# Optimization experiments

Hardware: AMD Instinct MI355X
Metric: run time of the kernel (lower is better)

Reference implementation:

```python
import jax, jax.numpy as jnp
import numpy as np

STD = 0.5      # wrapper's self.std used as the noise sampling std
EPS = 1e-12    # BERT LayerNorm eps
NOISE_SEED = 42


def setup_inputs() -> dict:
    key = jax.random.key(0)
    ks = jax.random.split(key, 8)
    B, S, H, V, P, T = 32, 512, 768, 30522, 512, 2
    return {
        "input_ids": jax.random.randint(ks[0], (B, S), 0, V, dtype=jnp.int32),
        "token_type_ids": jnp.zeros((B, S), dtype=jnp.int32),
        "importance_scores": jax.random.uniform(ks[1], (B, S), dtype=jnp.float32),
        "word_emb": jax.random.normal(ks[2], (V, H), dtype=jnp.float32) * 0.02,
        "pos_emb": jax.random.normal(ks[3], (P, H), dtype=jnp.float32) * 0.02,
        "type_emb": jax.random.normal(ks[4], (T, H), dtype=jnp.float32) * 0.02,
        "ln_gamma": jnp.ones((H,), dtype=jnp.float32),
        "ln_beta": jnp.zeros((H,), dtype=jnp.float32),
    }


def _layernorm(x, g, b):
    mu = x.mean(-1, keepdims=True)
    var = ((x - mu) ** 2).mean(-1, keepdims=True)
    return (x - mu) * jax.lax.rsqrt(var + EPS) * g + b


def reference(input_ids, token_type_ids, importance_scores, word_emb, pos_emb,
              type_emb, ln_gamma, ln_beta):
    B, S = input_ids.shape
    # BERT embeddings: word + position + token_type, then LayerNorm (dropout=eval/no-op)
    emb = word_emb[input_ids] + pos_emb[:S][None, :, :] + type_emb[token_type_ids]
    x = _layernorm(emb, ln_gamma, ln_beta)  # [B,S,H]

    # min-max normalize importance scores per sequence (inf handled as in original)
    smax = importance_scores.max(axis=1, keepdims=True)
    tmp = jnp.where(jnp.isinf(importance_scores), 99.0, importance_scores)
    smin = tmp.min(axis=1, keepdims=True)
    norm = (importance_scores - smin) / (smax - smin)
    norm = jnp.where(importance_scores.sum() == 0, importance_scores, norm)

    finite = jnp.isfinite(importance_scores)
    score = jnp.where(finite, norm, 0.0)      # -inf positions masked out below
    score = score.at[:, 0].set(1.0)           # CLS token forced to importance 1
    mask = finite.at[:, 0].set(True)

    # soft_suff: sigma = 1 - importance; noise ~ N(0, STD); x += noise * sigma * x
    sigma = (1.0 - score) * mask.astype(x.dtype)          # [B,S]
    noise = jax.random.normal(jax.random.key(NOISE_SEED), x.shape, dtype=x.dtype) * STD
    x = x + noise * sigma[:, :, None] * jax.lax.stop_gradient(x)
    return x
```

## Files before the change

kernel.cpp:

```cpp
#include <hip/hip_runtime.h>
#include <math.h>

#define Hh   768
#define Ss   512
#define Bb   32
#define NTOK (Bb * Ss)
#define NT   192

__device__ __forceinline__ void tfr(unsigned &x0, unsigned &x1, int r) {
  x0 += x1;
  x1 = (x1 << r) | (x1 >> (32 - r));
  x1 ^= x0;
}

__device__ __forceinline__ unsigned tf_bits_0_42(unsigned ctr) {
  const unsigned ks1 = 42u, ks2 = 0x1BD11BF0u;
  unsigned x0 = 0u, x1 = ctr + ks1;
  tfr(x0,x1,13); tfr(x0,x1,15); tfr(x0,x1,26); tfr(x0,x1,6);
  x0 += ks1; x1 += ks2 + 1u;
  tfr(x0,x1,17); tfr(x0,x1,29); tfr(x0,x1,16); tfr(x0,x1,24);
  x0 += ks2; x1 += 2u;
  tfr(x0,x1,13); tfr(x0,x1,15); tfr(x0,x1,26); tfr(x0,x1,6);
  x1 += ks1 + 3u;
  tfr(x0,x1,17); tfr(x0,x1,29); tfr(x0,x1,16); tfr(x0,x1,24);
  x0 += ks1; x1 += ks2 + 4u;
  tfr(x0,x1,13); tfr(x0,x1,15); tfr(x0,x1,26); tfr(x0,x1,6);
  x0 += ks2; x1 += 5u;
  return x0 ^ x1;
}

__device__ __forceinline__ float erfinv_bits(unsigned bits) {
  float f = __uint_as_float((bits >> 9) | 0x3F800000u) - 1.0f;
  const float LO = -0.99999994f;
  float x = fmaxf(LO, fmaf(f, 2.0f, LO));
  float w = -__logf(fmaf(-x, x, 1.0f));
  float p;
  if (w < 5.0f) {
    w -= 2.5f;
    p = 2.81022636e-08f;
    p = fmaf(p, w, 3.43273939e-07f);
    p = fmaf(p, w, -3.5233877e-06f);
    p = fmaf(p, w, -4.39150654e-06f);
    p = fmaf(p, w, 0.00021858087f);
    p = fmaf(p, w, -0.00125372503f);
    p = fmaf(p, w, -0.00417768164f);
    p = fmaf(p, w, 0.246640727f);
    p = fmaf(p, w, 1.50140941f);
  } else {
    w = sqrtf(w) - 3.0f;
    p = -0.000200214257f;
    p = fmaf(p, w, 0.000100950558f);
    p = fmaf(p, w, 0.00134934322f);
    p = fmaf(p, w, -0.00367342844f);
    p = fmaf(p, w, 0.00573950773f);
    p = fmaf(p, w, -0.0076224613f);
    p = fmaf(p, w, 0.00943887047f);
    p = fmaf(p, w, 1.00167406f);
    p = fmaf(p, w, 2.83297682f);
  }
  return p * x;
}

__global__ __launch_bounds__(512) void row_stats_kernel(
    const float* __restrict__ imp, float* __restrict__ ws) {
  int b = blockIdx.x;
  int tid = threadIdx.x;
  float v = imp[b * Ss + tid];
  float vmax = v;
  float vmin = isinf(v) ? 99.0f : v;
  float vsum = v;
  for (int o = 32; o > 0; o >>= 1) {
    vmax = fmaxf(vmax, __shfl_down(vmax, o));
    vmin = fminf(vmin, __shfl_down(vmin, o));
    vsum += __shfl_down(vsum, o);
  }
  __shared__ float smax[8], smin[8], ssum[8];
  int wave = tid >> 6, lane = tid & 63;
  if (lane == 0) { smax[wave] = vmax; smin[wave] = vmin; ssum[wave] = vsum; }
  __syncthreads();
  if (tid == 0) {
    float a = smax[0], m = smin[0], c = ssum[0];
    for (int w = 1; w < 8; ++w) {
      a = fmaxf(a, smax[w]); m = fminf(m, smin[w]); c += ssum[w];
    }
    ws[b] = a; ws[32 + b] = m; ws[64 + b] = c;
  }
}

__global__ __launch_bounds__(NT) void bert_embed_ln_noise_kernel(
    const int* __restrict__ ids, const int* __restrict__ tts,
    const float* __restrict__ imp,
    const float* __restrict__ wemb, const float* __restrict__ pemb,
    const float* __restrict__ temb, const float* __restrict__ gamma,
    const float* __restrict__ beta, const float* __restrict__ stats,
    float* __restrict__ out) {
  const int t = blockIdx.x;
  const int b = t >> 9;
  const int s = t & 511;
  const int tid = threadIdx.x;

  const int id = ids[t];
  const int tt = tts[t];
  const float4 wv = ((const float4*)(wemb + (size_t)id * Hh))[tid];
  const float4 pv = ((const float4*)(pemb + (size_t)s  * Hh))[tid];
  const float4 tv = ((const float4*)(temb + (size_t)tt * Hh))[tid];

  const float e0 = wv.x + pv.x + tv.x;
  const float e1 = wv.y + pv.y + tv.y;
  const float e2 = wv.z + pv.z + tv.z;
  const float e3 = wv.w + pv.w + tv.w;

  const unsigned base = (unsigned)t * Hh + 4u * (unsigned)tid;
  const unsigned r0 = tf_bits_0_42(base);
  const unsigned r1 = tf_bits_0_42(base + 1u);
  const unsigned r2 = tf_bits_0_42(base + 2u);
  const unsigned r3 = tf_bits_0_42(base + 3u);
  const float v0 = erfinv_bits(r0);
  const float v1 = erfinv_bits(r1);
  const float v2 = erfinv_bits(r2);
  const float v3 = erfinv_bits(r3);

  __shared__ float redm[3], redv[3];
  __shared__ float sh_ssc;
  const int wave = tid >> 6, lane = tid & 63;

  float ps = (e0 + e1) + (e2 + e3);
  #pragma unroll
  for (int o = 1; o < 64; o <<= 1) ps += __shfl_xor(ps, o);
  if (lane == 0) redm[wave] = ps;
  __syncthreads();
  const float mu = (redm[0] + redm[1] + redm[2]) * (1.0f / Hh);

  const float d0 = e0 - mu, d1 = e1 - mu, d2 = e2 - mu, d3 = e3 - mu;
  float pvv = (d0 * d0 + d1 * d1) + (d2 * d2 + d3 * d3);
  #pragma unroll
  for (int o = 1; o < 64; o <<= 1) pvv += __shfl_xor(pvv, o);
  if (lane == 0) redv[wave] = pvv;

  if (tid == 0) {
    float total = 0.0f;
    for (int w = 0; w < 32; ++w) total += stats[64 + w];
    const float score = imp[t];
    float sig = 0.0f;
    if (s != 0) {
      const bool fin = isfinite(score);
      const float mx = stats[b], mn = stats[32 + b];
      const float val = (total == 0.0f) ? score : (score - mn) / (mx - mn);
      sig = fin ? (1.0f - val) : 0.0f;
    }
    sh_ssc = sig * 0.70710677f;
  }
  __syncthreads();
  const float var = (redv[0] + redv[1] + redv[2]) * (1.0f / Hh);
  const float rstd = rsqrtf(var + 1e-12f);
  const float ssc = sh_ssc;

  const float4 g4 = ((const float4*)gamma)[tid];
  const float4 b4 = ((const float4*)beta)[tid];
  const float y0 = fmaf(d0 * rstd, g4.x, b4.x);
  const float y1 = fmaf(d1 * rstd, g4.y, b4.y);
  const float y2 = fmaf(d2 * rstd, g4.z, b4.z);
  const float y3 = fmaf(d3 * rstd, g4.w, b4.w);

  float4 o4;
  o4.x = fmaf(v0 * ssc, y0, y0);
  o4.y = fmaf(v1 * ssc, y1, y1);
  o4.z = fmaf(v2 * ssc, y2, y2);
  o4.w = fmaf(v3 * ssc, y3, y3);
  ((float4*)(out + (size_t)t * Hh))[tid] = o4;
}

extern "C" void kernel_launch(void* const* d_in, const int* in_sizes, int n_in,
                              void* d_out, int out_size, void* d_ws, size_t ws_size,
                              hipStream_t stream) {
  const int*   ids   = (const int*)d_in[0];
  const int*   tts   = (const int*)d_in[1];
  const float* imp   = (const float*)d_in[2];
  const float* wemb  = (const float*)d_in[3];
  const float* pemb  = (const float*)d_in[4];
  const float* temb  = (const float*)d_in[5];
  const float* gamma = (const float*)d_in[6];
  const float* beta  = (const float*)d_in[7];
  float* out   = (float*)d_out;
  float* stats = (float*)d_ws;

  row_stats_kernel<<<Bb, Ss, 0, stream>>>(imp, stats);
  bert_embed_ln_noise_kernel<<<NTOK, NT, 0, stream>>>(
      ids, tts, imp, wemb, pemb, temb, gamma, beta, stats, out);
}
```

Baseline: 173.6 us.

## Map one token per wavefront, precompute sigma, and make erfinv branchless

Restructures the main kernel so each 64-lane wavefront handles a whole token (12 elements per lane), packing four tokens per 256-thread block. LayerNorm reductions then use only wave shuffles, with no shared memory or __syncthreads. Per-token sigma moves into a separate small kernel that writes to workspace. The erfinv polynomial now evaluates both branches and selects one, avoiding divergence. The cost is an extra kernel launch and more live registers per thread.

```diff
diff --git a/kernel.cpp b/kernel.cpp
--- a/kernel.cpp
+++ b/kernel.cpp
@@ -5,7 +5,6 @@
 #define Ss   512
 #define Bb   32
 #define NTOK (Bb * Ss)
-#define NT   192
 
 __device__ __forceinline__ void tfr(unsigned &x0, unsigned &x1, int r) {
   x0 += x1;
@@ -34,30 +33,27 @@
   const float LO = -0.99999994f;
   float x = fmaxf(LO, fmaf(f, 2.0f, LO));
   float w = -__logf(fmaf(-x, x, 1.0f));
-  float p;
-  if (w < 5.0f) {
-    w -= 2.5f;
-    p = 2.81022636e-08f;
-    p = fmaf(p, w, 3.43273939e-07f);
-    p = fmaf(p, w, -3.5233877e-06f);
-    p = fmaf(p, w, -4.39150654e-06f);
-    p = fmaf(p, w, 0.00021858087f);
-    p = fmaf(p, w, -0.00125372503f);
-    p = fmaf(p, w, -0.00417768164f);
-    p = fmaf(p, w, 0.246640727f);
-    p = fmaf(p, w, 1.50140941f);
-  } else {
-    w = sqrtf(w) - 3.0f;
-    p = -0.000200214257f;
-    p = fmaf(p, w, 0.000100950558f);
-    p = fmaf(p, w, 0.00134934322f);
-    p = fmaf(p, w, -0.00367342844f);
-    p = fmaf(p, w, 0.00573950773f);
-    p = fmaf(p, w, -0.0076224613f);
-    p = fmaf(p, w, 0.00943887047f);
-    p = fmaf(p, w, 1.00167406f);
-    p = fmaf(p, w, 2.83297682f);
-  }
+  float wc = w - 2.5f;
+  float pc = 2.81022636e-08f;
+  pc = fmaf(pc, wc, 3.43273939e-07f);
+  pc = fmaf(pc, wc, -3.5233877e-06f);
+  pc = fmaf(pc, wc, -4.39150654e-06f);
+  pc = fmaf(pc, wc, 0.00021858087f);
+  pc = fmaf(pc, wc, -0.00125372503f);
+  pc = fmaf(pc, wc, -0.00417768164f);
+  pc = fmaf(pc, wc, 0.246640727f);
+  pc = fmaf(pc, wc, 1.50140941f);
+  float wt = __fsqrt_rn(w) - 3.0f;
+  float pt = -0.000200214257f;
+  pt = fmaf(pt, wt, 0.000100950558f);
+  pt = fmaf(pt, wt, 0.00134934322f);
+  pt = fmaf(pt, wt, -0.00367342844f);
+  pt = fmaf(pt, wt, 0.00573950773f);
+  pt = fmaf(pt, wt, -0.0076224613f);
+  pt = fmaf(pt, wt, 0.00943887047f);
+  pt = fmaf(pt, wt, 1.00167406f);
+  pt = fmaf(pt, wt, 2.83297682f);
+  float p = (w < 5.0f) ? pc : pt;
   return p * x;
 }
 
@@ -87,87 +83,100 @@
   }
 }
 
-__global__ __launch_bounds__(NT) void bert_embed_ln_noise_kernel(
+__global__ __launch_bounds__(256) void sigma_kernel(
+    const float* __restrict__ imp, float* __restrict__ ws) {
+  const int t = blockIdx.x * 256 + threadIdx.x;
+  const int b = t >> 9;
+  const int s = t & 511;
+  float total = 0.0f;
+  #pragma unroll
+  for (int w = 0; w < 32; ++w) total += ws[64 + w];
+  const float score = imp[t];
+  float sig = 0.0f;
+  if (s != 0) {
+    const bool fin = isfinite(score);
+    const float mx = ws[b], mn = ws[32 + b];
+    const float val = (total == 0.0f) ? score : (score - mn) / (mx - mn);
+    sig = fin ? (1.0f - val) : 0.0f;
+  }
+  ws[128 + t] = sig * 0.70710677f;
+}
+
+__global__ __launch_bounds__(256) void bert_embed_ln_noise_kernel(
     const int* __restrict__ ids, const int* __restrict__ tts,
-    const float* __restrict__ imp,
     const float* __restrict__ wemb, const float* __restrict__ pemb,
     const float* __restrict__ temb, const float* __restrict__ gamma,
-    const float* __restrict__ beta, const float* __restrict__ stats,
+    const float* __restrict__ beta, const float* __restrict__ ws,
     float* __restrict__ out) {
-  const int t = blockIdx.x;
+  const int wv   = threadIdx.x >> 6;
+  const int lane = threadIdx.x & 63;
+  const int t = (blockIdx.x << 2) + wv;
   const int b = t >> 9;
   const int s = t & 511;
-  const int tid = threadIdx.x;
+  (void)b;
 
   const int id = ids[t];
   const int tt = tts[t];
-  const float4 wv = ((const float4*)(wemb + (size_t)id * Hh))[tid];
-  const float4 pv = ((const float4*)(pemb + (size_t)s  * Hh))[tid];
-  const float4 tv = ((const float4*)(temb + (size_t)tt * Hh))[tid];
-
-  const float e0 = wv.x + pv.x + tv.x;
-  const float e1 = wv.y + pv.y + tv.y;
-  const float e2 = wv.z + pv.z + tv.z;
-  const float e3 = wv.w + pv.w + tv.w;
-
-  const unsigned base = (unsigned)t * Hh + 4u * (unsigned)tid;
-  const unsigned r0 = tf_bits_0_42(base);
-  const unsigned r1 = tf_bits_0_42(base + 1u);
-  const unsigned r2 = tf_bits_0_42(base + 2u);
-  const unsigned r3 = tf_bits_0_42(base + 3u);
-  const float v0 = erfinv_bits(r0);
-  const float v1 = erfinv_bits(r1);
-  const float v2 = erfinv_bits(r2);
-  const float v3 = erfinv_bits(r3);
-
-  __shared__ float redm[3], redv[3];
-  __shared__ float sh_ssc;
-  const int wave = tid >> 6, lane = tid & 63;
-
-  float ps = (e0 + e1) + (e2 + e3);
+  const float4* wr = (const float4*)(wemb + (size_t)id * Hh);
+  const float4* pr = (const float4*)(pemb + (size_t)s  * Hh);
+  const float4* tr = (const float4*)(temb + (size_t)tt * Hh);
+
+  float4 e[3];
+  #pragma unroll
+  for (int g = 0; g < 3; ++g) {
+    const float4 a = wr[lane + 64 * g];
+    const float4 p = pr[lane + 64 * g];
+    const float4 c = tr[lane + 64 * g];
+    e[g].x = a.x + p.x + c.x;
+    e[g].y = a.y + p.y + c.y;
+    e[g].z = a.z + p.z + c.z;
+    e[g].w = a.w + p.w + c.w;
+  }
+
+  float ps = ((e[0].x + e[0].y) + (e[0].z + e[0].w))
+           + ((e[1].x + e[1].y) + (e[1].z + e[1].w))
+           + ((e[2].x + e[2].y) + (e[2].z + e[2].w));
   #pragma unroll
   for (int o = 1; o < 64; o <<= 1) ps += __shfl_xor(ps, o);
-  if (lane == 0) redm[wave] = ps;
-  __syncthreads();
-  const float mu = (redm[0] + redm[1] + redm[2]) * (1.0f / Hh);
-
-  const float d0 = e0 - mu, d1 = e1 - mu, d2 = e2 - mu, d3 = e3 - mu;
-  float pvv = (d0 * d0 + d1 * d1) + (d2 * d2 + d3 * d3);
+  const float mu = ps * (1.0f / Hh);
+
+  float pvv = 0.0f;
+  #pragma unroll
+  for (int g = 0; g < 3; ++g) {
+    e[g].x -= mu; e[g].y -= mu; e[g].z -= mu; e[g].w -= mu;
+    pvv += (e[g].x * e[g].x + e[g].y * e[g].y)
+         + (e[g].z * e[g].z + e[g].w * e[g].w);
+  }
   #pragma unroll
   for (int o = 1; o < 64; o <<= 1) pvv += __shfl_xor(pvv, o);
-  if (lane == 0) redv[wave] = pvv;
-
-  if (tid == 0) {
-    float total = 0.0f;
-    for (int w = 0; w < 32; ++w) total += stats[64 + w];
-    const float score = imp[t];
-    float sig = 0.0f;
-    if (s != 0) {
-      const bool fin = isfinite(score);
-      const float mx = stats[b], mn = stats[32 + b];
-      const float val = (total == 0.0f) ? score : (score - mn) / (mx - mn);
-      sig = fin ? (1.0f - val) : 0.0f;
-    }
-    sh_ssc = sig * 0.70710677f;
-  }
-  __syncthreads();
-  const float var = (redv[0] + redv[1] + redv[2]) * (1.0f / Hh);
-  const float rstd = rsqrtf(var + 1e-12f);
-  const float ssc = sh_ssc;
-
-  const float4 g4 = ((const float4*)gamma)[tid];
-  const float4 b4 = ((const float4*)beta)[tid];
-  const float y0 = fmaf(d0 * rstd, g4.x, b4.x);
-  const float y1 = fmaf(d1 * rstd, g4.y, b4.y);
-  const float y2 = fmaf(d2 * rstd, g4.z, b4.z);
-  const float y3 = fmaf(d3 * rstd, g4.w, b4.w);
-
-  float4 o4;
-  o4.x = fmaf(v0 * ssc, y0, y0);
-  o4.y = fmaf(v1 * ssc, y1, y1);
-  o4.z = fmaf(v2 * ssc, y2, y2);
-  o4.w = fmaf(v3 * ssc, y3, y3);
-  ((float4*)(out + (size_t)t * Hh))[tid] = o4;
+  const float rstd = rsqrtf(pvv * (1.0f / Hh) + 1e-12f);
+  const float ssc = ws[128 + t];
+
+  const unsigned base = (unsigned)t * Hh + 4u * (unsigned)lane;
+  float4* op = (float4*)(out + (size_t)t * Hh);
+
+  #pragma unroll
+  for (int g = 0; g < 3; ++g) {
+    const float4 g4 = ((const float4*)gamma)[lane + 64 * g];
+    const float4 b4 = ((const float4*)beta )[lane + 64 * g];
+    const float y0 = fmaf(e[g].x * rstd, g4.x, b4.x);
+    const float y1 = fmaf(e[g].y * rstd, g4.y, b4.y);
+    const float y2 = fmaf(e[g].z * rstd, g4.z, b4.z);
+    const float y3 = fmaf(e[g].w * rstd, g4.w, b4.w);
+
+    const unsigned c0 = base + 256u * g;
+    const float n0 = erfinv_bits(tf_bits_0_42(c0));
+    const float n1 = erfinv_bits(tf_bits_0_42(c0 + 1u));
+    const float n2 = erfinv_bits(tf_bits_0_42(c0 + 2u));
+    const float n3 = erfinv_bits(tf_bits_0_42(c0 + 3u));
+
+    float4 o4;
+    o4.x = fmaf(n0 * ssc, y0, y0);
+    o4.y = fmaf(n1 * ssc, y1, y1);
+    o4.z = fmaf(n2 * ssc, y2, y2);
+    o4.w = fmaf(n3 * ssc, y3, y3);
+    op[lane + 64 * g] = o4;
+  }
 }
 
 extern "C" void kernel_launch(void* const* d_in, const int* in_sizes, int n_in,
@@ -182,9 +191,10 @@
   const float* gamma = (const float*)d_in[6];
   const float* beta  = (const float*)d_in[7];
   float* out   = (float*)d_out;
-  float* stats = (float*)d_ws;
-
-  row_stats_kernel<<<Bb, Ss, 0, stream>>>(imp, stats);
-  bert_embed_ln_noise_kernel<<<NTOK, NT, 0, stream>>>(
-      ids, tts, imp, wemb, pemb, temb, gamma, beta, stats, out);
-}
+  float* ws    = (float*)d_ws;
+
+  row_stats_kernel<<<Bb, Ss, 0, stream>>>(imp, ws);
+  sigma_kernel<<<NTOK / 256, 256, 0, stream>>>(imp, ws);
+  bert_embed_ln_noise_kernel<<<NTOK / 4, 256, 0, stream>>>(
+      ids, tts, wemb, pemb, temb, gamma, beta, ws, out);
+}
```

Result: no change. 176.5 us (+1.7%).
